# Kernel tuning notes

Measured on AMD Instinct MI355X. Metric: run time of the kernel, lower is better.

## Reference

```python
import jax, jax.numpy as jnp
import numpy as np

B, N, C, H = 4, 2048, 1024, 16
HD = C // H
SCALE = HD ** -0.5


def setup_inputs() -> dict:
    key = jax.random.key(0)
    k1, k2, k3, k4 = jax.random.split(key, 4)
    x = jax.random.normal(k1, (B, N, C), dtype=jnp.float32)
    # torch nn.Linear weights: [out, in]
    w_qkv = jax.random.normal(k2, (3 * C, C), dtype=jnp.float32) * (C ** -0.5)
    w_proj = jax.random.normal(k3, (C, C), dtype=jnp.float32) * (C ** -0.5)
    b_proj = jax.random.normal(k4, (C,), dtype=jnp.float32) * 0.01
    return {"x": x, "w_qkv": w_qkv, "w_proj": w_proj, "b_proj": b_proj}


def reference(x, w_qkv, w_proj, b_proj):
    Bx, Nx, Cx = x.shape
    # qkv projection: [B,N,3C] -> [3,B,H,N,HD]
    qkv = jnp.einsum('bnc,dc->bnd', x, w_qkv)
    qkv = qkv.reshape(Bx, Nx, 3, H, HD).transpose(2, 0, 3, 1, 4)
    q, k, v = qkv[0], qkv[1], qkv[2]
    attn = jnp.einsum('bhqd,bhkd->bhqk', q, k) * SCALE
    attn = jax.nn.softmax(attn, axis=-1)
    # dropout p=0.0 (eval/identity)
    out = jnp.einsum('bhqk,bhkd->bhqd', attn, v)
    out = out.transpose(0, 2, 1, 3).reshape(Bx, Nx, Cx)
    return jnp.einsum('bnc,dc->bnd', out, w_proj) + b_proj
```

## Files before the change

kernel.cpp:

```cpp
#include <hip/hip_runtime.h>


typedef float f32x2 __attribute__((ext_vector_type(2)));
typedef float f32x4 __attribute__((ext_vector_type(4)));
typedef float f32x16 __attribute__((ext_vector_type(16)));
typedef __bf16 bf16x8 __attribute__((ext_vector_type(8)));
typedef __bf16 bf16x4 __attribute__((ext_vector_type(4)));
typedef __bf16 bf16x2 __attribute__((ext_vector_type(2)));
typedef unsigned int u32;
typedef unsigned int u32x2 __attribute__((ext_vector_type(2)));

__device__ __forceinline__ void async16(const void* g, void* l) {
  __builtin_amdgcn_global_load_lds((const __attribute__((address_space(1))) unsigned int*)g,
                                   (__attribute__((address_space(3))) unsigned int*)l, 16, 0, 0);
}
__device__ __forceinline__ u32 cvtpk_bf16(float lo, float hi) {
  u32 r;
  asm("v_cvt_pk_bf16_f32 %0, %1, %2" : "=v"(r) : "v"(lo), "v"(hi));
  return r;
}
__device__ __forceinline__ void swap32(u32& a, u32& b) {
  asm volatile("v_permlane32_swap_b32 %0, %1" : "+v"(a), "+v"(b));
}
__device__ __forceinline__ float xmax64(float x) { return fmaxf(x, __shfl_xor(x, 32, 64)); }
__device__ __forceinline__ float xsum64(float x) { return x + __shfl_xor(x, 32, 64); }
__device__ __forceinline__ float exp2v(float x) { return __builtin_amdgcn_exp2f(x); }
__device__ __forceinline__ f32x2 pkmax(f32x2 a, f32x2 b) {
  return f32x2{ fmaxf(a.x, b.x), fmaxf(a.y, b.y) };
}

__global__ __launch_bounds__(256) void cast_to_bf16(const float* __restrict__ x,
                                                    const float* __restrict__ wq,
                                                    const float* __restrict__ wp,
                                                    __bf16* __restrict__ xo,
                                                    __bf16* __restrict__ wqo,
                                                    __bf16* __restrict__ wpo) {
  long i = (long)blockIdx.x * 256 + threadIdx.x;
  const float* s; __bf16* d; long j;
  if (i < 2097152L)      { s = x;  d = xo;  j = i; }
  else if (i < 2883584L) { s = wq; d = wqo; j = i - 2097152L; }
  else                   { s = wp; d = wpo; j = i - 2883584L; }
  float4 v = ((const float4*)s)[j];
  bf16x4 o = { (__bf16)v.x, (__bf16)v.y, (__bf16)v.z, (__bf16)v.w };
  ((bf16x4*)d)[j] = o;
}

template <int EPI>
__global__ __launch_bounds__(256) void gemm_bt(const __bf16* __restrict__ A,
                                               const __bf16* __restrict__ Bw,
                                               __bf16* __restrict__ Oq,
                                               float* __restrict__ Of,
                                               const float* __restrict__ bias) {
  const int tid = threadIdx.x;
  const int lane = tid & 63, w = tid >> 6;
  const int arow = lane & 15, agrp = lane >> 4;
  const int wm = w >> 1, wn = w & 1;
  const int bm = blockIdx.x, bn = blockIdx.y;
  __shared__ __bf16 As[128 * 32];
  __shared__ __bf16 Bs[128 * 32];
  f32x4 acc[4][4] = {};

  const int c0 = tid, c1 = tid + 256;
  const __bf16* Ag0 = A + ((size_t)(bm * 128 + (c0 >> 2)) << 10) + (c0 & 3) * 8;
  const __bf16* Ag1 = A + ((size_t)(bm * 128 + (c1 >> 2)) << 10) + (c1 & 3) * 8;
  const __bf16* Bg0 = Bw + ((size_t)(bn * 128 + (c0 >> 2)) << 10) + (c0 & 3) * 8;
  const __bf16* Bg1 = Bw + ((size_t)(bn * 128 + (c1 >> 2)) << 10) + (c1 & 3) * 8;

  for (int kt = 0; kt < 1024; kt += 32) {
    async16(Ag0 + kt, &As[c0 * 8]);
    async16(Ag1 + kt, &As[c1 * 8]);
    async16(Bg0 + kt, &Bs[c0 * 8]);
    async16(Bg1 + kt, &Bs[c1 * 8]);
    __syncthreads();
    bf16x8 af[4], bfr[4];
#pragma unroll
    for (int mi = 0; mi < 4; ++mi)
      af[mi] = *(const bf16x8*)&As[(wm * 64 + mi * 16 + arow) * 32 + agrp * 8];
#pragma unroll
    for (int ni = 0; ni < 4; ++ni)
      bfr[ni] = *(const bf16x8*)&Bs[(wn * 64 + ni * 16 + arow) * 32 + agrp * 8];
#pragma unroll
    for (int mi = 0; mi < 4; ++mi)
#pragma unroll
      for (int ni = 0; ni < 4; ++ni)
        acc[mi][ni] = __builtin_amdgcn_mfma_f32_16x16x32_bf16(af[mi], bfr[ni], acc[mi][ni], 0, 0, 0);
    __syncthreads();
  }

  const int rowb = bm * 128 + wm * 64 + agrp * 4;
  const int colb = bn * 128 + wn * 64 + arow;
  if (EPI == 0) {
#pragma unroll
    for (int mi = 0; mi < 4; ++mi) {
      const int row = rowb + mi * 16;
      const int bidx = row >> 11;
#pragma unroll
      for (int ni = 0; ni < 4; ++ni) {
        f32x4 v = acc[mi][ni];
        const int col = colb + ni * 16;
        const int which = col >> 10;
        const int h = (col >> 6) & 15;
        const int hd = col & 63;
        const float s = (which == 0) ? 0.18033688011112042f : 1.0f;
        __bf16* dst = Oq + ((size_t)which * 64 + bidx * 16 + h) * (size_t)(2048 * 64) + hd;
#pragma unroll
        for (int i = 0; i < 4; ++i)
          dst[(size_t)((row + i) & 2047) * 64] = (__bf16)(v[i] * s);
      }
    }
  } else {
#pragma unroll
    for (int mi = 0; mi < 4; ++mi) {
      const int row = rowb + mi * 16;
#pragma unroll
      for (int ni = 0; ni < 4; ++ni) {
        const int col = colb + ni * 16;
        const float bv = bias[col];
        f32x4 v = acc[mi][ni];
#pragma unroll
        for (int i = 0; i < 4; ++i)
          Of[(size_t)(row + i) * 1024 + col] = v[i] + bv;
      }
    }
  }
}

__global__ __launch_bounds__(256) void mhsa_attn(const __bf16* __restrict__ QKV,
                                                 __bf16* __restrict__ Out) {
  const int tid = threadIdx.x;
  const int lane = tid & 63, w = tid >> 6;
  const int blk = blockIdx.x;
  const int bh = blk & 63, qt = blk >> 6;
  const int lq = lane & 31, hi = lane >> 5;
  const int l7 = lane & 7;

  const size_t bhoff = (size_t)bh * (2048 * 64);
  const __bf16* Qp = QKV + bhoff;
  const __bf16* Kp = QKV + (size_t)(64 * 2048 * 64) + bhoff;
  const __bf16* Vp = QKV + (size_t)(128 * 2048 * 64) + bhoff;

  __shared__ char smem[32768];

  const int q0 = qt * 128 + w * 32;

  bf16x8 qf[4];
#pragma unroll
  for (int s = 0; s < 4; ++s)
    qf[s] = *(const bf16x8*)&Qp[(size_t)(q0 + lq) * 64 + s * 16 + hi * 8];

  f32x16 Oacc0 = 0.f, Oacc1 = 0.f;
  float m_run = -1e30f, l_run = 0.f;

  const int kr0 = tid >> 3, kc8 = tid & 7;
  const int kr1 = kr0 + 32;
  const int c8v = tid >> 5, k0v = (tid & 31) * 2;
  const int koff0 = (kr0 * 128 + kc8 * 16) ^ ((kr0 & 7) << 4);
  const int koff1 = (kr1 * 128 + kc8 * 16) ^ ((kr1 & 7) << 4);

  {
    bf16x8 kv0 = *(const bf16x8*)&Kp[(size_t)kr0 * 64 + kc8 * 8];
    bf16x8 kv1 = *(const bf16x8*)&Kp[(size_t)kr1 * 64 + kc8 * 8];
    bf16x8 v0 = *(const bf16x8*)&Vp[(size_t)k0v * 64 + c8v * 8];
    bf16x8 v1 = *(const bf16x8*)&Vp[(size_t)(k0v + 1) * 64 + c8v * 8];
    char* Kb = smem;
    char* Vb = smem + 8192;
    *(bf16x8*)(Kb + koff0) = kv0;
    *(bf16x8*)(Kb + koff1) = kv1;
#pragma unroll
    for (int j = 0; j < 8; ++j) {
      const int d = c8v * 8 + j;
      bf16x2 pr = { v0[j], v1[j] };
      *(bf16x2*)(Vb + ((d * 128 + k0v * 2) ^ ((d & 7) << 4))) = pr;
    }
  }
  __syncthreads();

  for (int t = 0; t < 32; ++t) {
    char* Kc = smem + (t & 1) * 16384;
    char* Vc = Kc + 8192;
    char* Kn = smem + ((t & 1) ^ 1) * 16384;
    char* Vn = Kn + 8192;

    bf16x8 kv0n, kv1n, v0n, v1n;
    const bool pf = (t < 31);
    if (pf) {
      const int ktn = (t + 1) * 64;
      kv0n = *(const bf16x8*)&Kp[(size_t)(ktn + kr0) * 64 + kc8 * 8];
      kv1n = *(const bf16x8*)&Kp[(size_t)(ktn + kr1) * 64 + kc8 * 8];
      v0n = *(const bf16x8*)&Vp[(size_t)(ktn + k0v) * 64 + c8v * 8];
      v1n = *(const bf16x8*)&Vp[(size_t)(ktn + k0v + 1) * 64 + c8v * 8];
    }

    f32x16 st0 = 0.f, st1 = 0.f;
    __builtin_amdgcn_s_setprio(1);
#pragma unroll
    for (int s = 0; s < 4; ++s) {
      bf16x8 kf = *(const bf16x8*)(Kc + lq * 128 + ((s * 32 + hi * 16) ^ (l7 << 4)));
      st0 = __builtin_amdgcn_mfma_f32_32x32x16_bf16(kf, qf[s], st0, 0, 0, 0);
    }
#pragma unroll
    for (int s = 0; s < 4; ++s) {
      bf16x8 kf = *(const bf16x8*)(Kc + (32 + lq) * 128 + ((s * 32 + hi * 16) ^ (l7 << 4)));
      st1 = __builtin_amdgcn_mfma_f32_32x32x16_bf16(kf, qf[s], st1, 0, 0, 0);
    }
    __builtin_amdgcn_s_setprio(0);

    f32x2 m2 = f32x2{ st0[0], st0[1] };
#pragma unroll
    for (int r = 1; r < 8; ++r) m2 = pkmax(m2, f32x2{ st0[2 * r], st0[2 * r + 1] });
#pragma unroll
    for (int r = 0; r < 8; ++r) m2 = pkmax(m2, f32x2{ st1[2 * r], st1[2 * r + 1] });
    float mx = xmax64(fmaxf(m2.x, m2.y));

    if (!__all(mx - m_run <= 8.f)) {
      const float mnew = fmaxf(m_run, mx);
      const float fs = exp2v(m_run - mnew);
      m_run = mnew;
      l_run *= fs;
#pragma unroll
      for (int r = 0; r < 16; ++r) { Oacc0[r] *= fs; Oacc1[r] *= fs; }
    }

    const float mb = m_run;
#pragma unroll
    for (int r = 0; r < 16; ++r) st0[r] = exp2v(st0[r] - mb);
#pragma unroll
    for (int r = 0; r < 16; ++r) st1[r] = exp2v(st1[r] - mb);
    f32x2 s2 = f32x2{ st0[0], st0[1] };
#pragma unroll
    for (int r = 1; r < 8; ++r) s2 += f32x2{ st0[2 * r], st0[2 * r + 1] };
#pragma unroll
    for (int r = 0; r < 8; ++r) s2 += f32x2{ st1[2 * r], st1[2 * r + 1] };
    l_run += xsum64(s2.x + s2.y);

    bf16x8 pa[4];
#pragma unroll
    for (int kb = 0; kb < 2; ++kb) {
      const f32x16& st = kb ? st1 : st0;
#pragma unroll
      for (int s16 = 0; s16 < 2; ++s16) {
        u32 A0 = cvtpk_bf16(st[8 * s16 + 0], st[8 * s16 + 1]);
        u32 B0 = cvtpk_bf16(st[8 * s16 + 4], st[8 * s16 + 5]);
        swap32(A0, B0);
        u32 A1 = cvtpk_bf16(st[8 * s16 + 2], st[8 * s16 + 3]);
        u32 B1 = cvtpk_bf16(st[8 * s16 + 6], st[8 * s16 + 7]);
        swap32(A1, B1);
        union { u32 wv[4]; bf16x8 v; } uu;
        uu.wv[0] = A0; uu.wv[1] = A1; uu.wv[2] = B0; uu.wv[3] = B1;
        pa[kb * 2 + s16] = uu.v;
      }
    }

    __builtin_amdgcn_s_setprio(1);
#pragma unroll
    for (int ks = 0; ks < 4; ++ks) {
      bf16x8 vf = *(const bf16x8*)(Vc + lq * 128 + ((ks * 32 + hi * 16) ^ (l7 << 4)));
      Oacc0 = __builtin_amdgcn_mfma_f32_32x32x16_bf16(vf, pa[ks], Oacc0, 0, 0, 0);
    }
#pragma unroll
    for (int ks = 0; ks < 4; ++ks) {
      bf16x8 vf = *(const bf16x8*)(Vc + (32 + lq) * 128 + ((ks * 32 + hi * 16) ^ (l7 << 4)));
      Oacc1 = __builtin_amdgcn_mfma_f32_32x32x16_bf16(vf, pa[ks], Oacc1, 0, 0, 0);
    }
    __builtin_amdgcn_s_setprio(0);

    if (pf) {
      *(bf16x8*)(Kn + koff0) = kv0n;
      *(bf16x8*)(Kn + koff1) = kv1n;
#pragma unroll
      for (int j = 0; j < 8; ++j) {
        const int d = c8v * 8 + j;
        bf16x2 pr = { v0n[j], v1n[j] };
        *(bf16x2*)(Vn + ((d * 128 + k0v * 2) ^ ((d & 7) << 4))) = pr;
      }
    }
    __syncthreads();
  }

  const float inv = 1.0f / l_run;
  const int b = bh >> 4, h = bh & 15;
  __bf16* orow = Out + ((size_t)(b * 2048 + q0 + lq)) * 1024 + h * 64;
#pragma unroll
  for (int db = 0; db < 2; ++db) {
    const f32x16& O = db ? Oacc1 : Oacc0;
#pragma unroll
    for (int rg = 0; rg < 4; ++rg) {
      u32 plo = cvtpk_bf16(O[rg * 4 + 0] * inv, O[rg * 4 + 1] * inv);
      u32 phi = cvtpk_bf16(O[rg * 4 + 2] * inv, O[rg * 4 + 3] * inv);
      u32x2 pk = { plo, phi };
      *(u32x2*)&orow[db * 32 + rg * 8 + hi * 4] = pk;
    }
  }
}

extern "C" void kernel_launch(void* const* d_in, const int* in_sizes, int n_in,
                              void* d_out, int out_size, void* d_ws, size_t ws_size,
                              hipStream_t stream) {
  const float* x  = (const float*)d_in[0];
  const float* wq = (const float*)d_in[1];
  const float* wp = (const float*)d_in[2];
  const float* bp = (const float*)d_in[3];
  char* ws = (char*)d_ws;

  __bf16* xo   = (__bf16*)(ws);
  __bf16* wqo  = (__bf16*)(ws + 16777216);
  __bf16* wpo  = (__bf16*)(ws + 23068672);
  __bf16* qkv  = (__bf16*)(ws + 25165824);
  __bf16* aout = xo;
  float* y = (float*)d_out;

  cast_to_bf16<<<12288, 256, 0, stream>>>(x, wq, wp, xo, wqo, wpo);
  gemm_bt<0><<<dim3(64, 24), 256, 0, stream>>>(xo, wqo, qkv, nullptr, nullptr);
  mhsa_attn<<<1024, 256, 0, stream>>>(qkv, aout);
  gemm_bt<1><<<dim3(64, 8), 256, 0, stream>>>(aout, wpo, nullptr, y, bp);
}
```

Measured before the change: 202.4 us.

## Process two 32-row query tiles per wave in attention to reuse K/V fragments

Each wave now handles 64 query rows (two independent 32-row groups with separate softmax state) instead of 32, so each block covers 256 queries and the grid halves to 512 blocks. Each K and V fragment read from LDS now feeds two MFMAs, halving LDS traffic and global K/V loads per query. The cost is higher register pressure (four score and four output accumulators), which may lower occupancy, and fewer blocks to spread across the CUs.

Result: slower. 222.6 us (+10.0%).

```diff
diff --git a/kernel.cpp b/kernel.cpp
--- a/kernel.cpp
+++ b/kernel.cpp
@@ -125,6 +125,54 @@
   }
 }
 
+__device__ __forceinline__ void softmax_pa(f32x16& st0, f32x16& st1, f32x16& O0, f32x16& O1,
+                                           float& m_run, float& l_run, bf16x8* pa) {
+  f32x2 m2 = f32x2{ st0[0], st0[1] };
+#pragma unroll
+  for (int r = 1; r < 8; ++r) m2 = pkmax(m2, f32x2{ st0[2 * r], st0[2 * r + 1] });
+#pragma unroll
+  for (int r = 0; r < 8; ++r) m2 = pkmax(m2, f32x2{ st1[2 * r], st1[2 * r + 1] });
+  float mx = xmax64(fmaxf(m2.x, m2.y));
+
+  if (!__all(mx - m_run <= 8.f)) {
+    const float mnew = fmaxf(m_run, mx);
+    const float fs = exp2v(m_run - mnew);
+    m_run = mnew;
+    l_run *= fs;
+#pragma unroll
+    for (int r = 0; r < 16; ++r) { O0[r] *= fs; O1[r] *= fs; }
+  }
+
+  const float mb = m_run;
+#pragma unroll
+  for (int r = 0; r < 16; ++r) st0[r] = exp2v(st0[r] - mb);
+#pragma unroll
+  for (int r = 0; r < 16; ++r) st1[r] = exp2v(st1[r] - mb);
+  f32x2 s2 = f32x2{ st0[0], st0[1] };
+#pragma unroll
+  for (int r = 1; r < 8; ++r) s2 += f32x2{ st0[2 * r], st0[2 * r + 1] };
+#pragma unroll
+  for (int r = 0; r < 8; ++r) s2 += f32x2{ st1[2 * r], st1[2 * r + 1] };
+  l_run += xsum64(s2.x + s2.y);
+
+#pragma unroll
+  for (int kb = 0; kb < 2; ++kb) {
+    const f32x16& st = kb ? st1 : st0;
+#pragma unroll
+    for (int s16 = 0; s16 < 2; ++s16) {
+      u32 A0 = cvtpk_bf16(st[8 * s16 + 0], st[8 * s16 + 1]);
+      u32 B0 = cvtpk_bf16(st[8 * s16 + 4], st[8 * s16 + 5]);
+      swap32(A0, B0);
+      u32 A1 = cvtpk_bf16(st[8 * s16 + 2], st[8 * s16 + 3]);
+      u32 B1 = cvtpk_bf16(st[8 * s16 + 6], st[8 * s16 + 7]);
+      swap32(A1, B1);
+      union { u32 wv[4]; bf16x8 v; } uu;
+      uu.wv[0] = A0; uu.wv[1] = A1; uu.wv[2] = B0; uu.wv[3] = B1;
+      pa[kb * 2 + s16] = uu.v;
+    }
+  }
+}
+
 __global__ __launch_bounds__(256) void mhsa_attn(const __bf16* __restrict__ QKV,
                                                  __bf16* __restrict__ Out) {
   const int tid = threadIdx.x;
@@ -141,15 +189,17 @@
 
   __shared__ char smem[32768];
 
-  const int q0 = qt * 128 + w * 32;
-
-  bf16x8 qf[4];
-#pragma unroll
-  for (int s = 0; s < 4; ++s)
-    qf[s] = *(const bf16x8*)&Qp[(size_t)(q0 + lq) * 64 + s * 16 + hi * 8];
-
-  f32x16 Oacc0 = 0.f, Oacc1 = 0.f;
-  float m_run = -1e30f, l_run = 0.f;
+  const int q0 = qt * 256 + w * 64;
+
+  bf16x8 qfA[4], qfB[4];
+#pragma unroll
+  for (int s = 0; s < 4; ++s) {
+    qfA[s] = *(const bf16x8*)&Qp[(size_t)(q0 + lq) * 64 + s * 16 + hi * 8];
+    qfB[s] = *(const bf16x8*)&Qp[(size_t)(q0 + 32 + lq) * 64 + s * 16 + hi * 8];
+  }
+
+  f32x16 OA0 = 0.f, OA1 = 0.f, OB0 = 0.f, OB1 = 0.f;
+  float mA = -1e30f, lA = 0.f, mB = -1e30f, lB = 0.f;
 
   const int kr0 = tid >> 3, kc8 = tid & 7;
   const int kr1 = kr0 + 32;
@@ -191,76 +241,38 @@
       v1n = *(const bf16x8*)&Vp[(size_t)(ktn + k0v + 1) * 64 + c8v * 8];
     }
 
-    f32x16 st0 = 0.f, st1 = 0.f;
+    f32x16 sA0 = 0.f, sA1 = 0.f, sB0 = 0.f, sB1 = 0.f;
     __builtin_amdgcn_s_setprio(1);
 #pragma unroll
     for (int s = 0; s < 4; ++s) {
       bf16x8 kf = *(const bf16x8*)(Kc + lq * 128 + ((s * 32 + hi * 16) ^ (l7 << 4)));
-      st0 = __builtin_amdgcn_mfma_f32_32x32x16_bf16(kf, qf[s], st0, 0, 0, 0);
+      sA0 = __builtin_amdgcn_mfma_f32_32x32x16_bf16(kf, qfA[s], sA0, 0, 0, 0);
+      sB0 = __builtin_amdgcn_mfma_f32_32x32x16_bf16(kf, qfB[s], sB0, 0, 0, 0);
     }
 #pragma unroll
     for (int s = 0; s < 4; ++s) {
       bf16x8 kf = *(const bf16x8*)(Kc + (32 + lq) * 128 + ((s * 32 + hi * 16) ^ (l7 << 4)));
-      st1 = __builtin_amdgcn_mfma_f32_32x32x16_bf16(kf, qf[s], st1, 0, 0, 0);
+      sA1 = __builtin_amdgcn_mfma_f32_32x32x16_bf16(kf, qfA[s], sA1, 0, 0, 0);
+      sB1 = __builtin_amdgcn_mfma_f32_32x32x16_bf16(kf, qfB[s], sB1, 0, 0, 0);
     }
     __builtin_amdgcn_s_setprio(0);
 
-    f32x2 m2 = f32x2{ st0[0], st0[1] };
-#pragma unroll
-    for (int r = 1; r < 8; ++r) m2 = pkmax(m2, f32x2{ st0[2 * r], st0[2 * r + 1] });
-#pragma unroll
-    for (int r = 0; r < 8; ++r) m2 = pkmax(m2, f32x2{ st1[2 * r], st1[2 * r + 1] });
-    float mx = xmax64(fmaxf(m2.x, m2.y));
-
-    if (!__all(mx - m_run <= 8.f)) {
-      const float mnew = fmaxf(m_run, mx);
-      const float fs = exp2v(m_run - mnew);
-      m_run = mnew;
-      l_run *= fs;
-#pragma unroll
-      for (int r = 0; r < 16; ++r) { Oacc0[r] *= fs; Oacc1[r] *= fs; }
-    }
-
-    const float mb = m_run;
-#pragma unroll
-    for (int r = 0; r < 16; ++r) st0[r] = exp2v(st0[r] - mb);
-#pragma unroll
-    for (int r = 0; r < 16; ++r) st1[r] = exp2v(st1[r] - mb);
-    f32x2 s2 = f32x2{ st0[0], st0[1] };
-#pragma unroll
-    for (int r = 1; r < 8; ++r) s2 += f32x2{ st0[2 * r], st0[2 * r + 1] };
-#pragma unroll
-    for (int r = 0; r < 8; ++r) s2 += f32x2{ st1[2 * r], st1[2 * r + 1] };
-    l_run += xsum64(s2.x + s2.y);
-
-    bf16x8 pa[4];
-#pragma unroll
-    for (int kb = 0; kb < 2; ++kb) {
-      const f32x16& st = kb ? st1 : st0;
-#pragma unroll
-      for (int s16 = 0; s16 < 2; ++s16) {
-        u32 A0 = cvtpk_bf16(st[8 * s16 + 0], st[8 * s16 + 1]);
-        u32 B0 = cvtpk_bf16(st[8 * s16 + 4], st[8 * s16 + 5]);
-        swap32(A0, B0);
-        u32 A1 = cvtpk_bf16(st[8 * s16 + 2], st[8 * s16 + 3]);
-        u32 B1 = cvtpk_bf16(st[8 * s16 + 6], st[8 * s16 + 7]);
-        swap32(A1, B1);
-        union { u32 wv[4]; bf16x8 v; } uu;
-        uu.wv[0] = A0; uu.wv[1] = A1; uu.wv[2] = B0; uu.wv[3] = B1;
-        pa[kb * 2 + s16] = uu.v;
-      }
-    }
+    bf16x8 paA[4], paB[4];
+    softmax_pa(sA0, sA1, OA0, OA1, mA, lA, paA);
+    softmax_pa(sB0, sB1, OB0, OB1, mB, lB, paB);
 
     __builtin_amdgcn_s_setprio(1);
 #pragma unroll
     for (int ks = 0; ks < 4; ++ks) {
       bf16x8 vf = *(const bf16x8*)(Vc + lq * 128 + ((ks * 32 + hi * 16) ^ (l7 << 4)));
-      Oacc0 = __builtin_amdgcn_mfma_f32_32x32x16_bf16(vf, pa[ks], Oacc0, 0, 0, 0);
+      OA0 = __builtin_amdgcn_mfma_f32_32x32x16_bf16(vf, paA[ks], OA0, 0, 0, 0);
+      OB0 = __builtin_amdgcn_mfma_f32_32x32x16_bf16(vf, paB[ks], OB0, 0, 0, 0);
     }
 #pragma unroll
     for (int ks = 0; ks < 4; ++ks) {
       bf16x8 vf = *(const bf16x8*)(Vc + (32 + lq) * 128 + ((ks * 32 + hi * 16) ^ (l7 << 4)));
-      Oacc1 = __builtin_amdgcn_mfma_f32_32x32x16_bf16(vf, pa[ks], Oacc1, 0, 0, 0);
+      OA1 = __builtin_amdgcn_mfma_f32_32x32x16_bf16(vf, paA[ks], OA1, 0, 0, 0);
+      OB1 = __builtin_amdgcn_mfma_f32_32x32x16_bf16(vf, paB[ks], OB1, 0, 0, 0);
     }
     __builtin_amdgcn_s_setprio(0);
 
@@ -277,18 +289,21 @@
     __syncthreads();
   }
 
-  const float inv = 1.0f / l_run;
   const int b = bh >> 4, h = bh & 15;
-  __bf16* orow = Out + ((size_t)(b * 2048 + q0 + lq)) * 1024 + h * 64;
-#pragma unroll
-  for (int db = 0; db < 2; ++db) {
-    const f32x16& O = db ? Oacc1 : Oacc0;
-#pragma unroll
-    for (int rg = 0; rg < 4; ++rg) {
-      u32 plo = cvtpk_bf16(O[rg * 4 + 0] * inv, O[rg * 4 + 1] * inv);
-      u32 phi = cvtpk_bf16(O[rg * 4 + 2] * inv, O[rg * 4 + 3] * inv);
-      u32x2 pk = { plo, phi };
-      *(u32x2*)&orow[db * 32 + rg * 8 + hi * 4] = pk;
+#pragma unroll
+  for (int g = 0; g < 2; ++g) {
+    const float inv = 1.0f / (g ? lB : lA);
+    __bf16* orow = Out + ((size_t)(b * 2048 + q0 + g * 32 + lq)) * 1024 + h * 64;
+#pragma unroll
+    for (int db = 0; db < 2; ++db) {
+      const f32x16& O = g ? (db ? OB1 : OB0) : (db ? OA1 : OA0);
+#pragma unroll
+      for (int rg = 0; rg < 4; ++rg) {
+        u32 plo = cvtpk_bf16(O[rg * 4 + 0] * inv, O[rg * 4 + 1] * inv);
+        u32 phi = cvtpk_bf16(O[rg * 4 + 2] * inv, O[rg * 4 + 3] * inv);
+        u32x2 pk = { plo, phi };
+        *(u32x2*)&orow[db * 32 + rg * 8 + hi * 4] = pk;
+      }
     }
   }
 }
@@ -311,6 +326,6 @@
 
   cast_to_bf16<<<12288, 256, 0, stream>>>(x, wq, wp, xo, wqo, wpo);
   gemm_bt<0><<<dim3(64, 24), 256, 0, stream>>>(xo, wqo, qkv, nullptr, nullptr);
-  mhsa_attn<<<1024, 256, 0, stream>>>(qkv, aout);
+  mhsa_attn<<<512, 256, 0, stream>>>(qkv, aout);
   gemm_bt<1><<<dim3(64, 8), 256, 0, stream>>>(aout, wpo, nullptr, y, bp);
 }
```
